# Performance work log

Hardware: AMD Instinct MI355X
Metric: run time of the kernel (lower is better)

The kernel has to match this reference:

```python
import jax, jax.numpy as jnp
import numpy as np

B, CIN, COUT, N, R = 4, 32, 64, 65536, 32
PAD = 0.1
NEG_SLOPE = 0.1


def _norm_coords(coords):
    # coords [B,3,N] in [-1,1]; map to continuous voxel space [0, R-1]
    return jnp.clip((coords / (1.0 + PAD) + 1.0) * 0.5 * (R - 1), 0.0, R - 1)


def scatter_mean(feat, coords):
    # feat [B,C,N], coords [B,3,N] -> voxel grid [B,C,R,R,R]
    b, c, n = feat.shape
    nc = _norm_coords(coords)
    idx = jnp.clip(jnp.floor(nc + 0.5), 0, R - 1).astype(jnp.int32)  # nearest voxel
    flat = (idx[:, 0] * R + idx[:, 1]) * R + idx[:, 2]               # [B,N]
    seg = (flat + jnp.arange(b, dtype=jnp.int32)[:, None] * (R ** 3)).reshape(-1)
    f = feat.transpose(0, 2, 1).reshape(b * n, c)
    sums = jax.ops.segment_sum(f, seg, num_segments=b * R ** 3)
    cnt = jax.ops.segment_sum(jnp.ones((b * n,), feat.dtype), seg, num_segments=b * R ** 3)
    mean = sums / jnp.maximum(cnt, 1.0)[:, None]
    return mean.reshape(b, R, R, R, c).transpose(0, 4, 1, 2, 3)


def trilinear_sample(grid, coords):
    # grid [B,C,R,R,R], coords [B,3,N] -> point features [B,C,N]
    b, c = grid.shape[:2]
    n = coords.shape[-1]
    nc = _norm_coords(coords)                      # [B,3,N]
    lo = jnp.floor(nc).astype(jnp.int32)
    lo = jnp.clip(lo, 0, R - 1)
    hi = jnp.minimum(lo + 1, R - 1)
    frac = nc - lo.astype(nc.dtype)                # [B,3,N]
    gflat = grid.reshape(b, c, R ** 3).transpose(0, 2, 1)  # [B, R^3, C]

    def corner(ix, iy, iz):
        fi = (ix * R + iy) * R + iz                # [B,N]
        return jnp.take_along_axis(gflat, fi[..., None], axis=1)  # [B,N,C]

    fx, fy, fz = frac[:, 0], frac[:, 1], frac[:, 2]
    x0, y0, z0 = lo[:, 0], lo[:, 1], lo[:, 2]
    x1, y1, z1 = hi[:, 0], hi[:, 1], hi[:, 2]
    w = lambda a: a[..., None]
    out = (corner(x0, y0, z0) * w((1 - fx) * (1 - fy) * (1 - fz))
           + corner(x0, y0, z1) * w((1 - fx) * (1 - fy) * fz)
           + corner(x0, y1, z0) * w((1 - fx) * fy * (1 - fz))
           + corner(x0, y1, z1) * w((1 - fx) * fy * fz)
           + corner(x1, y0, z0) * w(fx * (1 - fy) * (1 - fz))
           + corner(x1, y0, z1) * w(fx * (1 - fy) * fz)
           + corner(x1, y1, z0) * w(fx * fy * (1 - fz))
           + corner(x1, y1, z1) * w(fx * fy * fz))
    return out.transpose(0, 2, 1)                  # [B,C,N]


def conv3d(x, w, b):
    y = jax.lax.conv_general_dilated(x, w, (1, 1, 1), 'SAME',
                                     dimension_numbers=('NCDHW', 'OIDHW', 'NCDHW'))
    return y + b[None, :, None, None, None]


def leaky(x):
    return jnp.where(x >= 0, x, NEG_SLOPE * x)


def setup_inputs() -> dict:
    key = jax.random.key(0)
    ks = jax.random.split(key, 6)
    features = jax.random.normal(ks[0], (B, CIN, N), jnp.float32)
    inputs = jax.random.uniform(ks[1], (B, 3, N), jnp.float32) * 2.0 - 1.0  # coords in [-1,1]
    w_mlp = jax.random.normal(ks[2], (COUT, CIN), jnp.float32) * 0.05
    b_mlp = jnp.zeros((COUT,), jnp.float32)
    w_conv1 = jax.random.normal(ks[3], (COUT, CIN, 3, 3, 3), jnp.float32) * 0.05
    b_conv1 = jnp.zeros((COUT,), jnp.float32)
    w_conv2 = jax.random.normal(ks[4], (COUT, COUT, 3, 3, 3), jnp.float32) * 0.05
    b_conv2 = jnp.zeros((COUT,), jnp.float32)
    return {"features": features, "inputs": inputs, "w_mlp": w_mlp, "b_mlp": b_mlp,
            "w_conv1": w_conv1, "b_conv1": b_conv1, "w_conv2": w_conv2, "b_conv2": b_conv2}


def reference(features, inputs, w_mlp, b_mlp, w_conv1, b_conv1, w_conv2, b_conv2):
    # First PVConv layer: voxelize point features (scatter-mean)
    voxel_in = scatter_mean(features, inputs)                     # [B,CIN,R,R,R]
    # point branch: Conv1d(k=1) + ReLU (mlp=False path, norm=None)
    point_feature = jax.nn.relu(jnp.einsum('oc,bcn->bon', w_mlp, features) + b_mlp[None, :, None])
    # voxel branch: DoubleConv = (conv3d -> leaky_relu) x 2, layer_order 'cna' with norm=None
    v = leaky(conv3d(voxel_in, w_conv1, b_conv1))
    voxel_feature = leaky(conv3d(v, w_conv2, b_conv2))            # [B,COUT,R,R,R]
    # fuse point feature: trilinear devoxelization gather + add
    sampled = trilinear_sample(voxel_feature, inputs)             # [B,COUT,N]
    point_out = point_feature + sampled
    return (point_out, voxel_feature)
```

## Files before the change

### kernel.cpp

```cpp
#include <hip/hip_runtime.h>

typedef unsigned short ushort_t;
typedef unsigned int uint_t;
typedef __attribute__((ext_vector_type(4))) float f32x4;
typedef __attribute__((ext_vector_type(16))) float f32x16;
typedef __attribute__((ext_vector_type(4))) unsigned int u32x4;
typedef __attribute__((ext_vector_type(8))) short short8;

#define R3 32768
#define NPTS 65536

__device__ __forceinline__ float bf_lo(uint_t u) { return __uint_as_float(u << 16); }
__device__ __forceinline__ float bf_hi(uint_t u) { return __uint_as_float(u & 0xffff0000u); }
__device__ __forceinline__ ushort_t f2b(float f) {
    uint_t u = __float_as_uint(f);
    u += 0x7fffu + ((u >> 16) & 1u);
    return (ushort_t)(u >> 16);
}
__device__ __forceinline__ float normc(float c) {
    float v = (c / 1.1f + 1.0f) * 0.5f * 31.0f;
    return fminf(fmaxf(v, 0.0f), 31.0f);
}

__global__ __launch_bounds__(256) void k_vid(const float* __restrict__ coords,
                                             int* __restrict__ vid,
                                             uint_t* __restrict__ hist) {
    int gid = blockIdx.x * 256 + threadIdx.x;
    int b = gid >> 16, n = gid & 65535;
    const float* cp = coords + (size_t)b * 3 * NPTS + n;
    int ix = (int)floorf(normc(cp[0]) + 0.5f);
    int iy = (int)floorf(normc(cp[NPTS]) + 0.5f);
    int iz = (int)floorf(normc(cp[2 * NPTS]) + 0.5f);
    ix = min(max(ix, 0), 31); iy = min(max(iy, 0), 31); iz = min(max(iz, 0), 31);
    int v = b * R3 + ((ix * 32 + iy) * 32 + iz);
    vid[gid] = v;
    atomicAdd(hist + v, 1u);
}

__global__ __launch_bounds__(256) void k_scanA(const uint_t* __restrict__ hist,
                                               uint_t* __restrict__ excl,
                                               uint_t* __restrict__ bsum) {
    __shared__ uint_t sh[256];
    int t = threadIdx.x;
    int base = blockIdx.x * 1024 + t * 4;
    uint_t v0 = hist[base], v1 = hist[base + 1], v2 = hist[base + 2], v3 = hist[base + 3];
    uint_t s = v0 + v1 + v2 + v3;
    sh[t] = s;
    __syncthreads();
    uint_t x = s;
    for (int off = 1; off < 256; off <<= 1) {
        uint_t y = (t >= off) ? sh[t - off] : 0u;
        __syncthreads();
        x += y;
        sh[t] = x;
        __syncthreads();
    }
    uint_t e = x - s;
    excl[base] = e;
    excl[base + 1] = e + v0;
    excl[base + 2] = e + v0 + v1;
    excl[base + 3] = e + v0 + v1 + v2;
    if (t == 255) bsum[blockIdx.x] = x;
}

__global__ __launch_bounds__(128) void k_scanB(uint_t* __restrict__ bsum,
                                               uint_t* __restrict__ boff) {
    __shared__ uint_t sh[128];
    int t = threadIdx.x;
    uint_t s = bsum[t];
    sh[t] = s;
    __syncthreads();
    uint_t x = s;
    for (int off = 1; off < 128; off <<= 1) {
        uint_t y = (t >= off) ? sh[t - off] : 0u;
        __syncthreads();
        x += y;
        sh[t] = x;
        __syncthreads();
    }
    boff[t] = x - s;
}

__global__ __launch_bounds__(256) void k_scanC(uint_t* __restrict__ excl,
                                               const uint_t* __restrict__ boff,
                                               uint_t* __restrict__ cursor) {
    int i = blockIdx.x * 256 + threadIdx.x;
    uint_t v = excl[i] + boff[i >> 10];
    excl[i] = v;
    cursor[i] = v;
}

__global__ __launch_bounds__(256) void k_scatfeat(const float* __restrict__ feat,
                                                  const int* __restrict__ vid,
                                                  uint_t* __restrict__ cursor,
                                                  ushort_t* __restrict__ sorted) {
    int gid = blockIdx.x * 256 + threadIdx.x;
    int b = gid >> 16, n = gid & 65535;
    int v = vid[gid];
    uint_t slot = atomicAdd(cursor + v, 1u);
    const float* f = feat + (size_t)b * 32 * NPTS + n;
    ushort_t* dst = sorted + (size_t)slot * 32;
#pragma unroll
    for (int q = 0; q < 4; ++q) {
        u32x4 val;
#pragma unroll
        for (int j = 0; j < 4; ++j) {
            float a = f[(size_t)(q * 8 + j * 2) * NPTS];
            float c = f[(size_t)(q * 8 + j * 2 + 1) * NPTS];
            val[j] = (uint_t)f2b(a) | ((uint_t)f2b(c) << 16);
        }
        *(u32x4*)(dst + q * 8) = val;
    }
}

__global__ __launch_bounds__(256) void k_reduce(const ushort_t* __restrict__ sorted,
                                                const uint_t* __restrict__ start,
                                                const uint_t* __restrict__ hist,
                                                ushort_t* __restrict__ mean_cl) {
    int v = blockIdx.x * 256 + threadIdx.x;
    uint_t s = start[v], c = hist[v];
    float acc[32];
#pragma unroll
    for (int i = 0; i < 32; ++i) acc[i] = 0.0f;
    for (uint_t i = 0; i < c; ++i) {
        const u32x4* p = (const u32x4*)(sorted + (size_t)(s + i) * 32);
#pragma unroll
        for (int q = 0; q < 4; ++q) {
            u32x4 val = p[q];
#pragma unroll
            for (int j = 0; j < 4; ++j) {
                acc[q * 8 + j * 2] += bf_lo(val[j]);
                acc[q * 8 + j * 2 + 1] += bf_hi(val[j]);
            }
        }
    }
    float inv = 1.0f / fmaxf((float)c, 1.0f);
    ushort_t* dst = mean_cl + (size_t)v * 32;
#pragma unroll
    for (int q = 0; q < 4; ++q) {
        u32x4 val;
#pragma unroll
        for (int j = 0; j < 4; ++j)
            val[j] = (uint_t)f2b(acc[q * 8 + j * 2] * inv) |
                     ((uint_t)f2b(acc[q * 8 + j * 2 + 1] * inv) << 16);
        *(u32x4*)(dst + q * 8) = val;
    }
}

__global__ __launch_bounds__(256) void k_wpack(const float* __restrict__ w1,
                                               const float* __restrict__ w2,
                                               ushort_t* __restrict__ Wp1,
                                               ushort_t* __restrict__ Wp2) {
    int t = blockIdx.x * 256 + threadIdx.x;
    if (t < 55296) {
        int dz = t / 18432, r = t % 18432;
        int kb = r >> 9, o = (r >> 3) & 63, ke = r & 7;
        int k = kb * 8 + ke, ci = k & 31, n9 = k >> 5;
        Wp1[t] = f2b(w1[(o * 32 + ci) * 27 + n9 * 3 + dz]);
    } else if (t < 165888) {
        int u = t - 55296;
        int dz = u / 36864, r = u % 36864;
        int kb = r >> 9, o = (r >> 3) & 63, ke = r & 7;
        int k = kb * 8 + ke, ci = k & 63, n9 = k >> 6;
        Wp2[u] = f2b(w2[(o * 64 + ci) * 27 + n9 * 3 + dz]);
    }
}

template <int CB, bool WRITE_CF>
__global__ __launch_bounds__(256, 4) void k_conv(const ushort_t* __restrict__ in_b16,
                                                 const ushort_t* __restrict__ Wp,
                                                 const float* __restrict__ bias,
                                                 ushort_t* __restrict__ out_cl,
                                                 float* __restrict__ out_cf) {
    constexpr int CI = CB * 8;
    constexpr int CHUNKS = CB * 10 * 19;
    constexpr int CPW = (CHUNKS + 255) / 256;
    constexpr int CHUNKS_PAD = CPW * 256;
    __shared__ union ShU {
        ushort_t T[CHUNKS_PAD * 8];
        float S[64][133];
    } sh;
    int tid = threadIdx.x, bid = blockIdx.x;
    int zh = bid & 1, ys = (bid >> 1) & 3, x = (bid >> 3) & 31, b = bid >> 8;
    int y0 = ys * 8, z0 = zh * 16;
    int lane = tid & 63, wv = tid >> 6;

    int soff[CPW];
    bool vld[CPW];
#pragma unroll
    for (int i = 0; i < CPW; ++i) {
        int c = (wv * CPW + i) * 64 + lane;
        int zz = c % 19, t1 = c / 19, yy = t1 % 10, cb = t1 / 10;
        int gy = y0 + yy - 1, gz = z0 + zz - 1;
        vld[i] = (c < CHUNKS) & ((unsigned)gy < 32u) & ((unsigned)gz < 32u);
        soff[i] = (gy * 32 + gz) * CI + cb * 8;
    }
    const ushort_t* inb = in_b16 + (size_t)b * R3 * CI;

    u32x4 sreg[CPW];
    auto stage_load = [&](int dx) {
        int gx = x + dx - 1;
        bool xok = (unsigned)gx < 32u;
        const ushort_t* base = inb + (size_t)gx * (1024 * CI);
#pragma unroll
        for (int i = 0; i < CPW; ++i) {
            u32x4 z4 = {0u, 0u, 0u, 0u};
            sreg[i] = (xok && vld[i]) ? *(const u32x4*)(base + soff[i]) : z4;
        }
    };
    auto stage_write = [&]() {
#pragma unroll
        for (int i = 0; i < CPW; ++i)
            *(u32x4*)(&sh.T[((wv * CPW + i) * 64 + lane) * 8]) = sreg[i];
    };

    int nq = wv & 1, mq = wv >> 1;
    int l31 = lane & 31, lh = lane >> 5;
    int o = nq * 32 + l31;
    int ya0 = mq * 4 + (l31 >> 4);
    int ya1 = ya0 + 2;
    int za = l31 & 15;

    f32x16 acc0, acc1;
#pragma unroll
    for (int i = 0; i < 16; ++i) { acc0[i] = 0.0f; acc1[i] = 0.0f; }

    stage_load(0);
    stage_write();
    __syncthreads();
#pragma unroll
    for (int dx = 0; dx < 3; ++dx) {
        if (dx < 2) stage_load(dx + 1);
        const ushort_t* Tp = &sh.T[0];
        const ushort_t* wpB = Wp + (size_t)o * 8;
#pragma unroll
        for (int dz = 0; dz < 3; ++dz)
#pragma unroll
            for (int dy = 0; dy < 3; ++dy)
#pragma unroll
                for (int cbp = 0; cbp < CB / 2; ++cbp) {
                    int cb = cbp * 2 + lh;
                    const ushort_t* tb = Tp + (size_t)cb * (10 * 19 * 8);
                    short8 a0 = *(const short8*)(tb + ((ya0 + dy) * 19 + za + dz) * 8);
                    short8 a1 = *(const short8*)(tb + ((ya1 + dy) * 19 + za + dz) * 8);
                    int kb = (dx * 3 + dy) * CB + cb;
                    short8 bw = *(const short8*)(wpB + (size_t)(dz * 9 * CB + kb) * 512);
                    acc0 = __builtin_amdgcn_mfma_f32_32x32x16_bf16(a0, bw, acc0, 0, 0, 0);
                    acc1 = __builtin_amdgcn_mfma_f32_32x32x16_bf16(a1, bw, acc1, 0, 0, 0);
                }
        __syncthreads();
        if (dx < 2) {
            stage_write();
            __syncthreads();
        }
    }

    float bia = bias[o];
#pragma unroll
    for (int i = 0; i < 2; ++i) {
        int mbase = (mq * 2 + i) * 32 + lh * 4;
#pragma unroll
        for (int rq = 0; rq < 4; ++rq) {
            f32x4 v4;
#pragma unroll
            for (int j = 0; j < 4; ++j) {
                float v = (i ? acc1[rq * 4 + j] : acc0[rq * 4 + j]) + bia;
                v4[j] = (v >= 0.0f) ? v : 0.1f * v;
            }
            *(f32x4*)(&sh.S[o][mbase + rq * 8]) = v4;
        }
    }
    __syncthreads();

    {
        int vl = tid >> 1, oh = tid & 1;
        int y = vl >> 4, z = vl & 15;
        ushort_t* dst =
            out_cl + ((size_t)(b * R3 + x * 1024 + (y0 + y) * 32 + z0 + z)) * 64 + oh * 32;
#pragma unroll
        for (int q = 0; q < 4; ++q) {
            u32x4 w;
#pragma unroll
            for (int j4 = 0; j4 < 4; ++j4) {
                int oo = oh * 32 + q * 8 + j4 * 2;
                w[j4] = (uint_t)f2b(sh.S[oo][vl]) | ((uint_t)f2b(sh.S[oo + 1][vl]) << 16);
            }
            *(u32x4*)(dst + q * 8) = w;
        }
    }
    if (WRITE_CF) {
        int oo = tid >> 2, zq = tid & 3;
        float* dp = out_cf + (size_t)(b * 64 + oo) * R3 + x * 1024 + y0 * 32 + z0 + zq * 4;
#pragma unroll
        for (int y = 0; y < 8; ++y)
            *(f32x4*)(dp + y * 32) = *(const f32x4*)(&sh.S[oo][y * 16 + zq * 4]);
    }
}

__global__ __launch_bounds__(256) void k_point(const float* __restrict__ feat,
                                               const float* __restrict__ coords,
                                               const float* __restrict__ w_mlp,
                                               const float* __restrict__ b_mlp,
                                               const ushort_t* __restrict__ vf,
                                               float* __restrict__ out) {
    __shared__ int vox_s[64][8];
    __shared__ float wgt_s[64][8];
    __shared__ float S[64][65];
    int tid = threadIdx.x;
    int b = blockIdx.x >> 10;
    int p0 = (blockIdx.x & 1023) * 64;

    {
        int p = tid & 63, cpair = tid >> 6;
        const float* cp = coords + (size_t)b * 3 * NPTS + p0 + p;
        float nx = normc(cp[0]), ny = normc(cp[NPTS]), nz = normc(cp[2 * NPTS]);
        int x0 = min(max((int)floorf(nx), 0), 31);
        int y0 = min(max((int)floorf(ny), 0), 31);
        int z0 = min(max((int)floorf(nz), 0), 31);
        float fx = nx - (float)x0, fy = ny - (float)y0, fz = nz - (float)z0;
        int x1 = min(x0 + 1, 31), y1 = min(y0 + 1, 31), z1 = min(z0 + 1, 31);
#pragma unroll
        for (int j = 0; j < 2; ++j) {
            int c = cpair * 2 + j;
            int xi = (c & 4) ? x1 : x0, yi = (c & 2) ? y1 : y0, zi = (c & 1) ? z1 : z0;
            float wc = ((c & 4) ? fx : 1.0f - fx) * ((c & 2) ? fy : 1.0f - fy) *
                       ((c & 1) ? fz : 1.0f - fz);
            vox_s[p][c] = (xi * 32 + yi) * 32 + zi;
            wgt_s[p][c] = wc;
        }
    }
    __syncthreads();

    int lane = tid & 63, wv = tid >> 6;
    {
        const ushort_t* vfb = vf + (size_t)b * R3 * 64 + lane;
        for (int t = 0; t < 16; ++t) {
            int p = wv * 16 + t;
            float s = 0.0f;
#pragma unroll
            for (int c = 0; c < 8; ++c) {
                int vox = vox_s[p][c];
                float wc = wgt_s[p][c];
                uint_t raw = (uint_t)vfb[(size_t)vox * 64];
                s = fmaf(wc, __uint_as_float(raw << 16), s);
            }
            S[p][lane] = s;
        }
    }
    __syncthreads();

    {
        int o0 = __builtin_amdgcn_readfirstlane(wv) * 16;
        const float* fb = feat + (size_t)b * 32 * NPTS + p0 + lane;
        float ft[32];
#pragma unroll
        for (int ci = 0; ci < 32; ++ci) ft[ci] = fb[(size_t)ci * NPTS];
        float* ob = out + ((size_t)b * 64 + o0) * NPTS + p0 + lane;
#pragma unroll
        for (int oi = 0; oi < 16; ++oi) {
            float m = b_mlp[o0 + oi];
            const float* wrow = w_mlp + (size_t)(o0 + oi) * 32;
#pragma unroll
            for (int ci = 0; ci < 32; ++ci) m = fmaf(wrow[ci], ft[ci], m);
            m = fmaxf(m, 0.0f);
            ob[(size_t)oi * NPTS] = m + S[lane][o0 + oi];
        }
    }
}

extern "C" void kernel_launch(void* const* d_in, const int* in_sizes, int n_in,
                              void* d_out, int out_size, void* d_ws, size_t ws_size,
                              hipStream_t stream) {
    const float* feat   = (const float*)d_in[0];
    const float* coords = (const float*)d_in[1];
    const float* w_mlp  = (const float*)d_in[2];
    const float* b_mlp  = (const float*)d_in[3];
    const float* w_c1   = (const float*)d_in[4];
    const float* b_c1   = (const float*)d_in[5];
    const float* w_c2   = (const float*)d_in[6];
    const float* b_c2   = (const float*)d_in[7];

    float* out = (float*)d_out;
    float* point_out = out;
    float* vfeat = out + 16777216;

    ushort_t* sorted  = (ushort_t*)out;
    ushort_t* mean_cl = (ushort_t*)(out + 4194304);
    ushort_t* v_cl    = (ushort_t*)(out + 6291456);
    int*      vid     = (int*)(out + 10485760);
    uint_t*   hist    = (uint_t*)(out + 10747904);
    uint_t*   excl    = (uint_t*)(out + 10878976);
    uint_t*   cursor  = (uint_t*)(out + 11010048);
    uint_t*   bsum    = (uint_t*)(out + 11141120);
    uint_t*   boff    = (uint_t*)(out + 11141248);
    ushort_t* Wp1     = (ushort_t*)(out + 11141376);
    ushort_t* Wp2     = (ushort_t*)(out + 11169024);
    ushort_t* vf_cl   = (ushort_t*)d_ws;

    hipMemsetAsync(hist, 0, 131072 * 4, stream);
    k_wpack<<<648, 256, 0, stream>>>(w_c1, w_c2, Wp1, Wp2);
    k_vid<<<1024, 256, 0, stream>>>(coords, vid, hist);
    k_scanA<<<128, 256, 0, stream>>>(hist, excl, bsum);
    k_scanB<<<1, 128, 0, stream>>>(bsum, boff);
    k_scanC<<<512, 256, 0, stream>>>(excl, boff, cursor);
    k_scatfeat<<<1024, 256, 0, stream>>>(feat, vid, cursor, sorted);
    k_reduce<<<512, 256, 0, stream>>>(sorted, excl, hist, mean_cl);
    k_conv<4, false><<<1024, 256, 0, stream>>>(mean_cl, Wp1, b_c1, v_cl, (float*)nullptr);
    k_conv<8, true><<<1024, 256, 0, stream>>>(v_cl, Wp2, b_c2, vf_cl, vfeat);
    k_point<<<4096, 256, 0, stream>>>(feat, coords, w_mlp, b_mlp, vf_cl, point_out);
}
```

Measured before the change: 166.9 us.

## Compute two x-planes per conv block to reuse staged input slabs

```diff
diff --git a/kernel.cpp b/kernel.cpp
--- a/kernel.cpp
+++ b/kernel.cpp
@@ -167,7 +167,7 @@
 }
 
 template <int CB, bool WRITE_CF>
-__global__ __launch_bounds__(256, 4) void k_conv(const ushort_t* __restrict__ in_b16,
+__global__ __launch_bounds__(256, 2) void k_conv(const ushort_t* __restrict__ in_b16,
                                                  const ushort_t* __restrict__ Wp,
                                                  const float* __restrict__ bias,
                                                  ushort_t* __restrict__ out_cl,
@@ -181,8 +181,8 @@
         float S[64][133];
     } sh;
     int tid = threadIdx.x, bid = blockIdx.x;
-    int zh = bid & 1, ys = (bid >> 1) & 3, x = (bid >> 3) & 31, b = bid >> 8;
-    int y0 = ys * 8, z0 = zh * 16;
+    int zh = bid & 1, ys = (bid >> 1) & 3, xp = (bid >> 3) & 15, b = bid >> 7;
+    int y0 = ys * 8, z0 = zh * 16, x0 = xp * 2;
     int lane = tid & 63, wv = tid >> 6;
 
     int soff[CPW];
@@ -198,8 +198,8 @@
     const ushort_t* inb = in_b16 + (size_t)b * R3 * CI;
 
     u32x4 sreg[CPW];
-    auto stage_load = [&](int dx) {
-        int gx = x + dx - 1;
+    auto stage_load = [&](int pl) {
+        int gx = x0 - 1 + pl;
         bool xok = (unsigned)gx < 32u;
         const ushort_t* base = inb + (size_t)gx * (1024 * CI);
 #pragma unroll
@@ -214,87 +214,102 @@
             *(u32x4*)(&sh.T[((wv * CPW + i) * 64 + lane) * 8]) = sreg[i];
     };
 
-    int nq = wv & 1, mq = wv >> 1;
     int l31 = lane & 31, lh = lane >> 5;
-    int o = nq * 32 + l31;
-    int ya0 = mq * 4 + (l31 >> 4);
-    int ya1 = ya0 + 2;
+    int ya = wv * 2 + (l31 >> 4);
     int za = l31 & 15;
 
-    f32x16 acc0, acc1;
-#pragma unroll
-    for (int i = 0; i < 16; ++i) { acc0[i] = 0.0f; acc1[i] = 0.0f; }
+    f32x16 a00, a01, a10, a11;
+#pragma unroll
+    for (int i = 0; i < 16; ++i) { a00[i] = 0.f; a01[i] = 0.f; a10[i] = 0.f; a11[i] = 0.f; }
 
     stage_load(0);
     stage_write();
     __syncthreads();
 #pragma unroll
-    for (int dx = 0; dx < 3; ++dx) {
-        if (dx < 2) stage_load(dx + 1);
-        const ushort_t* Tp = &sh.T[0];
-        const ushort_t* wpB = Wp + (size_t)o * 8;
-#pragma unroll
-        for (int dz = 0; dz < 3; ++dz)
-#pragma unroll
-            for (int dy = 0; dy < 3; ++dy)
-#pragma unroll
-                for (int cbp = 0; cbp < CB / 2; ++cbp) {
-                    int cb = cbp * 2 + lh;
-                    const ushort_t* tb = Tp + (size_t)cb * (10 * 19 * 8);
-                    short8 a0 = *(const short8*)(tb + ((ya0 + dy) * 19 + za + dz) * 8);
-                    short8 a1 = *(const short8*)(tb + ((ya1 + dy) * 19 + za + dz) * 8);
-                    int kb = (dx * 3 + dy) * CB + cb;
-                    short8 bw = *(const short8*)(wpB + (size_t)(dz * 9 * CB + kb) * 512);
-                    acc0 = __builtin_amdgcn_mfma_f32_32x32x16_bf16(a0, bw, acc0, 0, 0, 0);
-                    acc1 = __builtin_amdgcn_mfma_f32_32x32x16_bf16(a1, bw, acc1, 0, 0, 0);
-                }
-        __syncthreads();
-        if (dx < 2) {
+    for (int p = 0; p < 4; ++p) {
+        if (p < 3) stage_load(p + 1);
+        int gx = x0 - 1 + p;
+        if ((unsigned)gx < 32u) {
+            const ushort_t* Tp = &sh.T[0];
+            const ushort_t* wpB = Wp + (size_t)l31 * 8;
+#pragma unroll
+            for (int dz = 0; dz < 3; ++dz)
+#pragma unroll
+                for (int dy = 0; dy < 3; ++dy)
+#pragma unroll
+                    for (int cbp = 0; cbp < CB / 2; ++cbp) {
+                        int cb = cbp * 2 + lh;
+                        const ushort_t* tb = Tp + (size_t)cb * (10 * 19 * 8);
+                        short8 a = *(const short8*)(tb + ((ya + dy) * 19 + za + dz) * 8);
+                        if (p < 3) {
+                            int kb = (p * 3 + dy) * CB + cb;
+                            const ushort_t* wk = wpB + (size_t)(dz * 9 * CB + kb) * 512;
+                            short8 w0 = *(const short8*)(wk);
+                            short8 w1 = *(const short8*)(wk + 256);
+                            a00 = __builtin_amdgcn_mfma_f32_32x32x16_bf16(a, w0, a00, 0, 0, 0);
+                            a01 = __builtin_amdgcn_mfma_f32_32x32x16_bf16(a, w1, a01, 0, 0, 0);
+                        }
+                        if (p >= 1) {
+                            int kb = ((p - 1) * 3 + dy) * CB + cb;
+                            const ushort_t* wk = wpB + (size_t)(dz * 9 * CB + kb) * 512;
+                            short8 w0 = *(const short8*)(wk);
+                            short8 w1 = *(const short8*)(wk + 256);
+                            a10 = __builtin_amdgcn_mfma_f32_32x32x16_bf16(a, w0, a10, 0, 0, 0);
+                            a11 = __builtin_amdgcn_mfma_f32_32x32x16_bf16(a, w1, a11, 0, 0, 0);
+                        }
+                    }
+        }
+        __syncthreads();
+        if (p < 3) {
             stage_write();
             __syncthreads();
         }
     }
 
-    float bia = bias[o];
-#pragma unroll
-    for (int i = 0; i < 2; ++i) {
-        int mbase = (mq * 2 + i) * 32 + lh * 4;
+    float bia0 = bias[l31], bia1 = bias[32 + l31];
+    auto emit = [&](const f32x16& lo, const f32x16& hi, int x) {
 #pragma unroll
         for (int rq = 0; rq < 4; ++rq) {
-            f32x4 v4;
+            f32x4 v0, v1;
 #pragma unroll
             for (int j = 0; j < 4; ++j) {
-                float v = (i ? acc1[rq * 4 + j] : acc0[rq * 4 + j]) + bia;
-                v4[j] = (v >= 0.0f) ? v : 0.1f * v;
+                float a = lo[rq * 4 + j] + bia0;
+                float c = hi[rq * 4 + j] + bia1;
+                v0[j] = (a >= 0.0f) ? a : 0.1f * a;
+                v1[j] = (c >= 0.0f) ? c : 0.1f * c;
             }
-            *(f32x4*)(&sh.S[o][mbase + rq * 8]) = v4;
-        }
-    }
-    __syncthreads();
-
-    {
-        int vl = tid >> 1, oh = tid & 1;
-        int y = vl >> 4, z = vl & 15;
-        ushort_t* dst =
-            out_cl + ((size_t)(b * R3 + x * 1024 + (y0 + y) * 32 + z0 + z)) * 64 + oh * 32;
-#pragma unroll
-        for (int q = 0; q < 4; ++q) {
-            u32x4 w;
-#pragma unroll
-            for (int j4 = 0; j4 < 4; ++j4) {
-                int oo = oh * 32 + q * 8 + j4 * 2;
-                w[j4] = (uint_t)f2b(sh.S[oo][vl]) | ((uint_t)f2b(sh.S[oo + 1][vl]) << 16);
+            int m = wv * 32 + lh * 4 + rq * 8;
+            *(f32x4*)(&sh.S[l31][m]) = v0;
+            *(f32x4*)(&sh.S[32 + l31][m]) = v1;
+        }
+        __syncthreads();
+        {
+            int vl = tid >> 1, oh = tid & 1;
+            int y = vl >> 4, z = vl & 15;
+            ushort_t* dst = out_cl +
+                ((size_t)(b * R3 + x * 1024 + (y0 + y) * 32 + z0 + z)) * 64 + oh * 32;
+#pragma unroll
+            for (int q = 0; q < 4; ++q) {
+                u32x4 w;
+#pragma unroll
+                for (int j4 = 0; j4 < 4; ++j4) {
+                    int oo = oh * 32 + q * 8 + j4 * 2;
+                    w[j4] = (uint_t)f2b(sh.S[oo][vl]) | ((uint_t)f2b(sh.S[oo + 1][vl]) << 16);
+                }
+                *(u32x4*)(dst + q * 8) = w;
             }
-            *(u32x4*)(dst + q * 8) = w;
-        }
-    }
-    if (WRITE_CF) {
-        int oo = tid >> 2, zq = tid & 3;
-        float* dp = out_cf + (size_t)(b * 64 + oo) * R3 + x * 1024 + y0 * 32 + z0 + zq * 4;
-#pragma unroll
-        for (int y = 0; y < 8; ++y)
-            *(f32x4*)(dp + y * 32) = *(const f32x4*)(&sh.S[oo][y * 16 + zq * 4]);
-    }
+        }
+        if (WRITE_CF) {
+            int oo = tid >> 2, zq = tid & 3;
+            float* dp = out_cf + (size_t)(b * 64 + oo) * R3 + x * 1024 + y0 * 32 + z0 + zq * 4;
+#pragma unroll
+            for (int y = 0; y < 8; ++y)
+                *(f32x4*)(dp + y * 32) = *(const f32x4*)(&sh.S[oo][y * 16 + zq * 4]);
+        }
+    };
+    emit(a00, a01, x0);
+    __syncthreads();
+    emit(a10, a11, x0 + 1);
 }
 
 __global__ __launch_bounds__(256) void k_point(const float* __restrict__ feat,
@@ -405,7 +420,7 @@
     k_scanC<<<512, 256, 0, stream>>>(excl, boff, cursor);
     k_scatfeat<<<1024, 256, 0, stream>>>(feat, vid, cursor, sorted);
     k_reduce<<<512, 256, 0, stream>>>(sorted, excl, hist, mean_cl);
-    k_conv<4, false><<<1024, 256, 0, stream>>>(mean_cl, Wp1, b_c1, v_cl, (float*)nullptr);
-    k_conv<8, true><<<1024, 256, 0, stream>>>(v_cl, Wp2, b_c2, vf_cl, vfeat);
+    k_conv<4, false><<<512, 256, 0, stream>>>(mean_cl, Wp1, b_c1, v_cl, (float*)nullptr);
+    k_conv<8, true><<<512, 256, 0, stream>>>(v_cl, Wp2, b_c2, vf_cl, vfeat);
     k_point<<<4096, 256, 0, stream>>>(feat, coords, w_mlp, b_mlp, vf_cl, point_out);
 }
```

New measurement: 176.4 us. +5.7%, slower.
